# Optimization experiments

Measured on AMD Instinct MI355X. Metric: run time of the kernel, lower is better.

The kernel has to match this reference:

```python
import math
import jax, jax.numpy as jnp
import numpy as np


def _unskew(X):
    # X: B x M x (M+L)  ->  B x M x L (each row i shifted left by i)
    B, M, MpL = X.shape
    L = MpL - M
    X = X.reshape(B, M * MpL)
    X = jnp.pad(X, ((0, 0), (0, M)))          # B x (M*(M+L)+M)
    X = X.reshape(B, M, MpL + 1)               # B x M x (M+L+1)
    return X[:, :, :L]


def _skew(X, pad_value):
    # X: B x M x L  ->  B x M x (M+L) (each row i shifted right by i)
    B, M, L = X.shape
    X = jnp.pad(X, ((0, 0), (0, 0), (0, M + 1)), constant_values=pad_value)
    X = X.reshape(B, -1)[:, :-M]               # B x (M*(M+L))
    return X.reshape(B, M, M + L)


def setup_inputs() -> dict:
    key = jax.random.key(0)
    k1, k2, k3, k4 = jax.random.split(key, 4)
    B, M, L, H = 128, 512, 1024, 64   # B = batch*heads, key len = M+L
    query = jax.random.normal(k1, (B, M, H), dtype=jnp.float32)
    key_t = jax.random.normal(k2, (B, M + L, H), dtype=jnp.float32)
    value = jax.random.normal(k3, (B, M + L, H), dtype=jnp.float32)
    key_pe = jax.random.normal(k4, (1, H, L), dtype=jnp.float32) * 0.02
    return {"query": query, "key": key_t, "value": value, "key_pe": key_pe}


def reference(query, key, value, key_pe):
    H = query.shape[-1]  # head_dim
    # content attention: B x M x (M+L), then unskew to relative coords B x M x L
    attn_cont = jnp.einsum('bmh,bnh->bmn', query, key)
    attn_cont = _unskew(attn_cont)
    # position attention: B x M x L (key_pe broadcasts over batch)
    attn_pos = jnp.einsum('bmh,xhl->bml', query, key_pe)
    attn = (attn_cont + attn_pos) / math.sqrt(H)
    attn = jax.nn.softmax(attn, axis=-1)
    # dropout p=0.0 -> identity
    attn_sk = _skew(attn, 0.0)                  # B x M x (M+L)
    out = jnp.einsum('bmn,bnh->bmh', attn_sk, value)
    return out
```

## Files before the change

### kernel.cpp

```cpp
#include <hip/hip_runtime.h>
#include <math.h>

typedef __bf16 bf16x8 __attribute__((ext_vector_type(8)));
typedef __bf16 bf16x4 __attribute__((ext_vector_type(4)));
typedef float  f32x4  __attribute__((ext_vector_type(4)));

constexpr int B_  = 128;
constexpr int M_  = 512;
constexpr int L_  = 1024;
constexpr int H_  = 64;
constexpr int KL_ = 1536;

constexpr int BM = 64;
constexpr int KT = 64;
constexpr int NT = 17;
constexpr int KS = 72;
constexpr int PPS = 256;
constexpr int PSS = 40;

constexpr int OFF_KS   = 0;
constexpr int OFF_VT   = 18432;
constexpr int OFF_PPOS = 36864;
constexpr int OFF_PS   = 69632;
constexpr int SMEM_BYTES = 79872;
constexpr int OFF_OBUF = 0;
constexpr int OFF_LSUM = 18432;
constexpr int OBS = 36;

#define MFMA16(A, B, C) __builtin_amdgcn_mfma_f32_16x16x32_bf16((A), (B), (C), 0, 0, 0)

__global__ __launch_bounds__(256, 2)
void seqattn_v5(const float* __restrict__ Q, const float* __restrict__ K,
                const float* __restrict__ V, const float* __restrict__ PE,
                float* __restrict__ O) {
  __shared__ alignas(16) char smem[SMEM_BYTES];
  __bf16* ksb  = (__bf16*)(smem + OFF_KS);
  __bf16* vtb  = (__bf16*)(smem + OFF_VT);
  __bf16* ppos = (__bf16*)(smem + OFF_PPOS);

  const int tid  = threadIdx.x;
  const int w    = tid >> 6;
  const int lane = tid & 63;
  const int nid  = lane & 15;
  const int qid  = lane >> 4;
  const int a    = w >> 1;
  const int c    = w & 1;
  const int b    = blockIdx.x;
  const int m0   = blockIdx.y * BM;
  const int swz  = qid << 4;

  __bf16* ps = (__bf16*)(smem + OFF_PS) + w * 32 * PSS;

  bf16x8 aq[2][2];
  #pragma unroll
  for (int it = 0; it < 2; ++it) {
    const float* qg = &Q[((size_t)b * M_ + m0 + 32 * a + 16 * it + nid) * H_];
    #pragma unroll
    for (int j = 0; j < 8; ++j) {
      aq[it][0][j] = (__bf16)qg[8 * qid + j];
      aq[it][1][j] = (__bf16)qg[32 + 8 * qid + j];
    }
  }

  f32x4 o[2][4];
  float lpart[2][4];
  #pragma unroll
  for (int it = 0; it < 2; ++it) {
    #pragma unroll
    for (int ht = 0; ht < 4; ++ht) o[it][ht] = (f32x4){0.f, 0.f, 0.f, 0.f};
    #pragma unroll
    for (int r = 0; r < 4; ++r) lpart[it][r] = 0.f;
  }

  const int krow = tid >> 2,  khq = (tid & 3) * 16;
  const int vj = (tid & 15) * 4, vh = (tid >> 4) * 4;

  const float* peg = &PE[(size_t)(8 * qid) * L_ + 32 * c + nid];

  f32x4 kr[4], vr[4];
  {
    const float* kg = &K[((size_t)b * KL_ + m0 + krow) * H_ + khq];
    kr[0] = *(const f32x4*)kg;       kr[1] = *(const f32x4*)(kg + 4);
    kr[2] = *(const f32x4*)(kg + 8); kr[3] = *(const f32x4*)(kg + 12);
    const float* vg = &V[((size_t)b * KL_ + m0 + vj) * H_ + vh];
    #pragma unroll
    for (int e = 0; e < 4; ++e) vr[e] = *(const f32x4*)(vg + e * H_);
  }
  {
    const f32x4 z = {0.f, 0.f, 0.f, 0.f};
    #pragma unroll
    for (int nt = 0; nt < 2; ++nt) {
      bf16x8 b0, b1;
      #pragma unroll
      for (int j = 0; j < 8; ++j) {
        b0[j] = (__bf16)peg[(size_t)j * L_ + 16 * nt];
        b1[j] = (__bf16)peg[(size_t)(32 + j) * L_ + 16 * nt];
      }
      const int colb = 32 * c + 16 * nt + nid;
      #pragma unroll
      for (int it = 0; it < 2; ++it) {
        f32x4 pp = MFMA16(aq[it][0], b0, z);
        pp = MFMA16(aq[it][1], b1, pp);
        #pragma unroll
        for (int r = 0; r < 4; ++r)
          ppos[(32 * a + 16 * it + 4 * qid + r) * PPS + (colb ^ swz)] = (__bf16)pp[r];
      }
    }
  }
  {
    bf16x8 x0, x1;
    #pragma unroll
    for (int j = 0; j < 4; ++j) {
      x0[j] = (__bf16)kr[0][j]; x0[4 + j] = (__bf16)kr[1][j];
      x1[j] = (__bf16)kr[2][j]; x1[4 + j] = (__bf16)kr[3][j];
    }
    *(bf16x8*)&ksb[krow * KS + khq] = x0;
    *(bf16x8*)&ksb[krow * KS + khq + 8] = x1;
    #pragma unroll
    for (int e = 0; e < 4; ++e) {
      bf16x4 y = {(__bf16)vr[0][e], (__bf16)vr[1][e], (__bf16)vr[2][e], (__bf16)vr[3][e]};
      *(bf16x4*)&vtb[(vh + e) * KS + vj] = y;
    }
  }
  __syncthreads();

  for (int t = 0; t < NT; ++t) {
    if (t < 16) {
      const int j1 = m0 + KT * (t + 1);
      const float* kg = &K[((size_t)b * KL_ + j1 + krow) * H_ + khq];
      kr[0] = *(const f32x4*)kg;       kr[1] = *(const f32x4*)(kg + 4);
      kr[2] = *(const f32x4*)(kg + 8); kr[3] = *(const f32x4*)(kg + 12);
      const float* vg = &V[((size_t)b * KL_ + j1 + vj) * H_ + vh];
      #pragma unroll
      for (int e = 0; e < 4; ++e) vr[e] = *(const f32x4*)(vg + e * H_);
    }
    bf16x8 pf[2][2];
    const int ch = t + 1;
    if (t < 15) {
      const float* pc = peg + ch * 64;
      #pragma unroll
      for (int nt = 0; nt < 2; ++nt) {
        #pragma unroll
        for (int j = 0; j < 8; ++j) {
          pf[nt][0][j] = (__bf16)pc[(size_t)j * L_ + 16 * nt];
          pf[nt][1][j] = (__bf16)pc[(size_t)(32 + j) * L_ + 16 * nt];
        }
      }
    }

    const __bf16* kst = ksb + (t & 1) * 64 * KS;
    const __bf16* vtt = vtb + (t & 1) * 64 * KS;
    const f32x4 z = {0.f, 0.f, 0.f, 0.f};

    f32x4 s[2][2];
    #pragma unroll
    for (int nt = 0; nt < 2; ++nt) {
      const __bf16* kb = &kst[(32 * c + 16 * nt + nid) * KS];
      const bf16x8 b0 = *(const bf16x8*)&kb[8 * qid];
      const bf16x8 b1 = *(const bf16x8*)&kb[32 + 8 * qid];
      #pragma unroll
      for (int it = 0; it < 2; ++it) {
        s[it][nt] = MFMA16(aq[it][0], b0, z);
        s[it][nt] = MFMA16(aq[it][1], b1, s[it][nt]);
      }
    }

    if (t < 15) {
      #pragma unroll
      for (int nt = 0; nt < 2; ++nt) {
        const int colb = ((ch & 3) << 6) + 32 * c + 16 * nt + nid;
        #pragma unroll
        for (int it = 0; it < 2; ++it) {
          f32x4 pp = MFMA16(aq[it][0], pf[nt][0], z);
          pp = MFMA16(aq[it][1], pf[nt][1], pp);
          #pragma unroll
          for (int r = 0; r < 4; ++r)
            ppos[(32 * a + 16 * it + 4 * qid + r) * PPS + (colb ^ swz)] = (__bf16)pp[r];
        }
      }
    }

    const bool edge = (t == 0) || (t == 16);
    #pragma unroll
    for (int it = 0; it < 2; ++it) {
      #pragma unroll
      for (int r = 0; r < 4; ++r) {
        const int il = 32 * a + 16 * it + 4 * qid + r;
        const int rb = il * PPS;
        #pragma unroll
        for (int nt = 0; nt < 2; ++nt) {
          const int l = KT * t + 32 * c + 16 * nt + nid - il;
          float p;
          if (!edge || (unsigned)l < 1024u) {
            const float pe = (float)ppos[rb + ((l & 255) ^ swz)];
            p = __expf((s[it][nt][r] + pe) * 0.125f);
          } else {
            p = 0.f;
          }
          lpart[it][r] += p;
          ps[(16 * it + 4 * qid + r) * PSS + 16 * nt + nid] = (__bf16)p;
        }
      }
    }

    #pragma unroll
    for (int it = 0; it < 2; ++it) {
      const bf16x8 ap = *(const bf16x8*)&ps[(16 * it + nid) * PSS + 8 * qid];
      #pragma unroll
      for (int ht = 0; ht < 4; ++ht) {
        o[it][ht] = MFMA16(ap, *(const bf16x8*)&vtt[(16 * ht + nid) * KS + 32 * c + 8 * qid],
                           o[it][ht]);
      }
    }

    if (t < 16) {
      __bf16* ksn = ksb + ((t + 1) & 1) * 64 * KS;
      __bf16* vtn = vtb + ((t + 1) & 1) * 64 * KS;
      bf16x8 x0, x1;
      #pragma unroll
      for (int j = 0; j < 4; ++j) {
        x0[j] = (__bf16)kr[0][j]; x0[4 + j] = (__bf16)kr[1][j];
        x1[j] = (__bf16)kr[2][j]; x1[4 + j] = (__bf16)kr[3][j];
      }
      *(bf16x8*)&ksn[krow * KS + khq] = x0;
      *(bf16x8*)&ksn[krow * KS + khq + 8] = x1;
      #pragma unroll
      for (int e = 0; e < 4; ++e) {
        bf16x4 y = {(__bf16)vr[0][e], (__bf16)vr[1][e], (__bf16)vr[2][e], (__bf16)vr[3][e]};
        *(bf16x4*)&vtn[(vh + e) * KS + vj] = y;
      }
    }
    __syncthreads();
  }

  float* lsum = (float*)(smem + OFF_LSUM);
  float* obuf = (float*)(smem + OFF_OBUF);

  #pragma unroll
  for (int it = 0; it < 2; ++it) {
    #pragma unroll
    for (int r = 0; r < 4; ++r) {
      float v = lpart[it][r];
      v += __shfl_xor(v, 1); v += __shfl_xor(v, 2);
      v += __shfl_xor(v, 4); v += __shfl_xor(v, 8);
      lpart[it][r] = v;
    }
  }
  if (nid == 0) {
    #pragma unroll
    for (int it = 0; it < 2; ++it)
      #pragma unroll
      for (int r = 0; r < 4; ++r)
        lsum[c * 64 + 32 * a + 16 * it + 4 * qid + r] = lpart[it][r];
  }
  if (c == 1) {
    #pragma unroll
    for (int it = 0; it < 2; ++it)
      #pragma unroll
      for (int ht = 0; ht < 4; ++ht)
        *(f32x4*)&obuf[(a * 64 + 16 * ht + nid) * OBS + 16 * it + 4 * qid] = o[it][ht];
  }
  __syncthreads();
  if (c == 0) {
    float inv[2][4];
    #pragma unroll
    for (int it = 0; it < 2; ++it)
      #pragma unroll
      for (int r = 0; r < 4; ++r) {
        const int row = 32 * a + 16 * it + 4 * qid + r;
        inv[it][r] = 1.f / (lsum[row] + lsum[64 + row]);
      }
    #pragma unroll
    for (int it = 0; it < 2; ++it) {
      #pragma unroll
      for (int ht = 0; ht < 4; ++ht) {
        f32x4 oo = o[it][ht] +
                   *(const f32x4*)&obuf[(a * 64 + 16 * ht + nid) * OBS + 16 * it + 4 * qid];
        #pragma unroll
        for (int r = 0; r < 4; ++r) {
          const int row = 32 * a + 16 * it + 4 * qid + r;
          O[((size_t)b * M_ + m0 + row) * H_ + 16 * ht + nid] = oo[r] * inv[it][r];
        }
      }
    }
  }
}

extern "C" void kernel_launch(void* const* d_in, const int* in_sizes, int n_in,
                              void* d_out, int out_size, void* d_ws, size_t ws_size,
                              hipStream_t stream) {
  const float* Q  = (const float*)d_in[0];
  const float* K  = (const float*)d_in[1];
  const float* V  = (const float*)d_in[2];
  const float* PE = (const float*)d_in[3];
  float* O = (float*)d_out;

  dim3 grid(B_, M_ / BM);
  hipLaunchKernelGGL(seqattn_v5, grid, dim3(256), 0, stream, Q, K, V, PE, O);
}
```

Baseline: 221.2 us.

## Compute transposed scores to keep softmax probabilities in registers for PV MFMA

Swaps the MFMA operand order so score tiles come out transposed, which puts each lane's probabilities in the layout the 16x16x16 bf16 MFMA A-operand expects. That removes the shared-memory round trip for P. K is now loaded straight from global into registers instead of being staged through LDS. The position table is stored pre-shifted with a new swizzle so it can be read as bf16x4 vectors. The smaller LDS footprint allows raising launch bounds to 3 blocks per CU, at the cost of more register pressure and less-coalesced K loads.

```diff
diff --git a/kernel.cpp b/kernel.cpp
--- a/kernel.cpp
+++ b/kernel.cpp
@@ -4,6 +4,7 @@
 typedef __bf16 bf16x8 __attribute__((ext_vector_type(8)));
 typedef __bf16 bf16x4 __attribute__((ext_vector_type(4)));
 typedef float  f32x4  __attribute__((ext_vector_type(4)));
+typedef short  s16x4  __attribute__((ext_vector_type(4)));
 
 constexpr int B_  = 128;
 constexpr int M_  = 512;
@@ -11,30 +12,31 @@
 constexpr int H_  = 64;
 constexpr int KL_ = 1536;
 
-constexpr int BM = 64;
-constexpr int KT = 64;
-constexpr int NT = 17;
-constexpr int KS = 72;
+constexpr int BM  = 64;
+constexpr int KT  = 64;
+constexpr int NT  = 17;
+constexpr int KS  = 72;
 constexpr int PPS = 256;
-constexpr int PSS = 40;
-
-constexpr int OFF_KS   = 0;
-constexpr int OFF_VT   = 18432;
-constexpr int OFF_PPOS = 36864;
-constexpr int OFF_PS   = 69632;
-constexpr int SMEM_BYTES = 79872;
+
+constexpr int OFF_VT   = 0;
+constexpr int OFF_PPOS = 18432;
+constexpr int SMEM_BYTES = 51200;
 constexpr int OFF_OBUF = 0;
 constexpr int OFF_LSUM = 18432;
 constexpr int OBS = 36;
 
-#define MFMA16(A, B, C) __builtin_amdgcn_mfma_f32_16x16x32_bf16((A), (B), (C), 0, 0, 0)
-
-__global__ __launch_bounds__(256, 2)
-void seqattn_v5(const float* __restrict__ Q, const float* __restrict__ K,
+#define MFMA32(A, B, C) __builtin_amdgcn_mfma_f32_16x16x32_bf16((A), (B), (C), 0, 0, 0)
+
+static __device__ __forceinline__ f32x4 mfma_pv(bf16x4 a, bf16x4 b, f32x4 c) {
+  return __builtin_amdgcn_mfma_f32_16x16x16bf16_1k(
+      __builtin_bit_cast(s16x4, a), __builtin_bit_cast(s16x4, b), c, 0, 0, 0);
+}
+
+__global__ __launch_bounds__(256, 3)
+void seqattn_v6(const float* __restrict__ Q, const float* __restrict__ K,
                 const float* __restrict__ V, const float* __restrict__ PE,
                 float* __restrict__ O) {
   __shared__ alignas(16) char smem[SMEM_BYTES];
-  __bf16* ksb  = (__bf16*)(smem + OFF_KS);
   __bf16* vtb  = (__bf16*)(smem + OFF_VT);
   __bf16* ppos = (__bf16*)(smem + OFF_PPOS);
 
@@ -47,9 +49,7 @@
   const int c    = w & 1;
   const int b    = blockIdx.x;
   const int m0   = blockIdx.y * BM;
-  const int swz  = qid << 4;
-
-  __bf16* ps = (__bf16*)(smem + OFF_PS) + w * 32 * PSS;
+  const int swzn = (nid & 7) << 2;
 
   bf16x8 aq[2][2];
   #pragma unroll
@@ -63,172 +63,186 @@
   }
 
   f32x4 o[2][4];
-  float lpart[2][4];
-  #pragma unroll
-  for (int it = 0; it < 2; ++it) {
+  float lpart[2] = {0.f, 0.f};
+  #pragma unroll
+  for (int it = 0; it < 2; ++it)
     #pragma unroll
     for (int ht = 0; ht < 4; ++ht) o[it][ht] = (f32x4){0.f, 0.f, 0.f, 0.f};
-    #pragma unroll
-    for (int r = 0; r < 4; ++r) lpart[it][r] = 0.f;
-  }
-
-  const int krow = tid >> 2,  khq = (tid & 3) * 16;
+
   const int vj = (tid & 15) * 4, vh = (tid >> 4) * 4;
 
   const float* peg = &PE[(size_t)(8 * qid) * L_ + 32 * c + nid];
 
-  f32x4 kr[4], vr[4];
+  bf16x8 ak[2][2];
+  #pragma unroll
+  for (int nt = 0; nt < 2; ++nt) {
+    const float* kg = &K[((size_t)b * KL_ + m0 + 32 * c + 16 * nt + nid) * H_ + 8 * qid];
+    const f32x4 k0 = *(const f32x4*)kg;
+    const f32x4 k1 = *(const f32x4*)(kg + 4);
+    const f32x4 k2 = *(const f32x4*)(kg + 32);
+    const f32x4 k3 = *(const f32x4*)(kg + 36);
+    #pragma unroll
+    for (int j = 0; j < 4; ++j) {
+      ak[nt][0][j] = (__bf16)k0[j]; ak[nt][0][4 + j] = (__bf16)k1[j];
+      ak[nt][1][j] = (__bf16)k2[j]; ak[nt][1][4 + j] = (__bf16)k3[j];
+    }
+  }
+  f32x4 vr[4];
   {
-    const float* kg = &K[((size_t)b * KL_ + m0 + krow) * H_ + khq];
-    kr[0] = *(const f32x4*)kg;       kr[1] = *(const f32x4*)(kg + 4);
-    kr[2] = *(const f32x4*)(kg + 8); kr[3] = *(const f32x4*)(kg + 12);
     const float* vg = &V[((size_t)b * KL_ + m0 + vj) * H_ + vh];
     #pragma unroll
     for (int e = 0; e < 4; ++e) vr[e] = *(const f32x4*)(vg + e * H_);
   }
   {
     const f32x4 z = {0.f, 0.f, 0.f, 0.f};
+    bf16x8 pf0[2][2];
+    #pragma unroll
+    for (int nt = 0; nt < 2; ++nt)
+      #pragma unroll
+      for (int j = 0; j < 8; ++j) {
+        pf0[nt][0][j] = (__bf16)peg[(size_t)j * L_ + 16 * nt];
+        pf0[nt][1][j] = (__bf16)peg[(size_t)(32 + j) * L_ + 16 * nt];
+      }
     #pragma unroll
     for (int nt = 0; nt < 2; ++nt) {
-      bf16x8 b0, b1;
-      #pragma unroll
-      for (int j = 0; j < 8; ++j) {
-        b0[j] = (__bf16)peg[(size_t)j * L_ + 16 * nt];
-        b1[j] = (__bf16)peg[(size_t)(32 + j) * L_ + 16 * nt];
-      }
-      const int colb = 32 * c + 16 * nt + nid;
       #pragma unroll
       for (int it = 0; it < 2; ++it) {
-        f32x4 pp = MFMA16(aq[it][0], b0, z);
-        pp = MFMA16(aq[it][1], b1, pp);
+        f32x4 pp = MFMA32(pf0[nt][0], aq[it][0], z);
+        pp = MFMA32(pf0[nt][1], aq[it][1], pp);
+        const int row = 32 * a + 16 * it + nid;
+        const int cb  = 32 * c + 16 * nt + 4 * qid + row;
         #pragma unroll
         for (int r = 0; r < 4; ++r)
-          ppos[(32 * a + 16 * it + 4 * qid + r) * PPS + (colb ^ swz)] = (__bf16)pp[r];
-      }
-    }
-  }
-  {
-    bf16x8 x0, x1;
-    #pragma unroll
-    for (int j = 0; j < 4; ++j) {
-      x0[j] = (__bf16)kr[0][j]; x0[4 + j] = (__bf16)kr[1][j];
-      x1[j] = (__bf16)kr[2][j]; x1[4 + j] = (__bf16)kr[3][j];
-    }
-    *(bf16x8*)&ksb[krow * KS + khq] = x0;
-    *(bf16x8*)&ksb[krow * KS + khq + 8] = x1;
-    #pragma unroll
-    for (int e = 0; e < 4; ++e) {
-      bf16x4 y = {(__bf16)vr[0][e], (__bf16)vr[1][e], (__bf16)vr[2][e], (__bf16)vr[3][e]};
-      *(bf16x4*)&vtb[(vh + e) * KS + vj] = y;
-    }
+          ppos[row * PPS + (((cb + r) & 255) ^ swzn)] = (__bf16)pp[r];
+      }
+    }
+  }
+  #pragma unroll
+  for (int e = 0; e < 4; ++e) {
+    bf16x4 y = {(__bf16)vr[0][e], (__bf16)vr[1][e], (__bf16)vr[2][e], (__bf16)vr[3][e]};
+    *(bf16x4*)&vtb[(vh + e) * KS + vj] = y;
   }
   __syncthreads();
 
   for (int t = 0; t < NT; ++t) {
+    bf16x4 pe4[2][2];
+    #pragma unroll
+    for (int it = 0; it < 2; ++it) {
+      const int row = 32 * a + 16 * it + nid;
+      #pragma unroll
+      for (int nt = 0; nt < 2; ++nt)
+        pe4[it][nt] = *(const bf16x4*)
+            &ppos[row * PPS + ((64 * (t & 3) + 32 * c + 16 * nt + 4 * qid) ^ swzn)];
+    }
+
+    bf16x8 akn[2][2];
     if (t < 16) {
       const int j1 = m0 + KT * (t + 1);
-      const float* kg = &K[((size_t)b * KL_ + j1 + krow) * H_ + khq];
-      kr[0] = *(const f32x4*)kg;       kr[1] = *(const f32x4*)(kg + 4);
-      kr[2] = *(const f32x4*)(kg + 8); kr[3] = *(const f32x4*)(kg + 12);
+      #pragma unroll
+      for (int nt = 0; nt < 2; ++nt) {
+        const float* kg = &K[((size_t)b * KL_ + j1 + 32 * c + 16 * nt + nid) * H_ + 8 * qid];
+        const f32x4 k0 = *(const f32x4*)kg;
+        const f32x4 k1 = *(const f32x4*)(kg + 4);
+        const f32x4 k2 = *(const f32x4*)(kg + 32);
+        const f32x4 k3 = *(const f32x4*)(kg + 36);
+        #pragma unroll
+        for (int j = 0; j < 4; ++j) {
+          akn[nt][0][j] = (__bf16)k0[j]; akn[nt][0][4 + j] = (__bf16)k1[j];
+          akn[nt][1][j] = (__bf16)k2[j]; akn[nt][1][4 + j] = (__bf16)k3[j];
+        }
+      }
       const float* vg = &V[((size_t)b * KL_ + j1 + vj) * H_ + vh];
       #pragma unroll
       for (int e = 0; e < 4; ++e) vr[e] = *(const f32x4*)(vg + e * H_);
     }
     bf16x8 pf[2][2];
-    const int ch = t + 1;
     if (t < 15) {
-      const float* pc = peg + ch * 64;
-      #pragma unroll
-      for (int nt = 0; nt < 2; ++nt) {
+      const float* pc = peg + (t + 1) * 64;
+      #pragma unroll
+      for (int nt = 0; nt < 2; ++nt)
         #pragma unroll
         for (int j = 0; j < 8; ++j) {
           pf[nt][0][j] = (__bf16)pc[(size_t)j * L_ + 16 * nt];
           pf[nt][1][j] = (__bf16)pc[(size_t)(32 + j) * L_ + 16 * nt];
         }
-      }
-    }
-
-    const __bf16* kst = ksb + (t & 1) * 64 * KS;
+    }
+
     const __bf16* vtt = vtb + (t & 1) * 64 * KS;
     const f32x4 z = {0.f, 0.f, 0.f, 0.f};
 
     f32x4 s[2][2];
     #pragma unroll
-    for (int nt = 0; nt < 2; ++nt) {
-      const __bf16* kb = &kst[(32 * c + 16 * nt + nid) * KS];
-      const bf16x8 b0 = *(const bf16x8*)&kb[8 * qid];
-      const bf16x8 b1 = *(const bf16x8*)&kb[32 + 8 * qid];
+    for (int nt = 0; nt < 2; ++nt)
       #pragma unroll
       for (int it = 0; it < 2; ++it) {
-        s[it][nt] = MFMA16(aq[it][0], b0, z);
-        s[it][nt] = MFMA16(aq[it][1], b1, s[it][nt]);
-      }
-    }
+        s[it][nt] = MFMA32(ak[nt][0], aq[it][0], z);
+        s[it][nt] = MFMA32(ak[nt][1], aq[it][1], s[it][nt]);
+      }
 
     if (t < 15) {
+      const int chb = 64 * ((t + 1) & 3);
       #pragma unroll
       for (int nt = 0; nt < 2; ++nt) {
-        const int colb = ((ch & 3) << 6) + 32 * c + 16 * nt + nid;
         #pragma unroll
         for (int it = 0; it < 2; ++it) {
-          f32x4 pp = MFMA16(aq[it][0], pf[nt][0], z);
-          pp = MFMA16(aq[it][1], pf[nt][1], pp);
+          f32x4 pp = MFMA32(pf[nt][0], aq[it][0], z);
+          pp = MFMA32(pf[nt][1], aq[it][1], pp);
+          const int row = 32 * a + 16 * it + nid;
+          const int cb  = chb + 32 * c + 16 * nt + 4 * qid + row;
           #pragma unroll
           for (int r = 0; r < 4; ++r)
-            ppos[(32 * a + 16 * it + 4 * qid + r) * PPS + (colb ^ swz)] = (__bf16)pp[r];
+            ppos[row * PPS + (((cb + r) & 255) ^ swzn)] = (__bf16)pp[r];
         }
       }
     }
 
     const bool edge = (t == 0) || (t == 16);
+    bf16x4 pa[2][2];
     #pragma unroll
     for (int it = 0; it < 2; ++it) {
-      #pragma unroll
-      for (int r = 0; r < 4; ++r) {
-        const int il = 32 * a + 16 * it + 4 * qid + r;
-        const int rb = il * PPS;
-        #pragma unroll
-        for (int nt = 0; nt < 2; ++nt) {
-          const int l = KT * t + 32 * c + 16 * nt + nid - il;
+      const int row = 32 * a + 16 * it + nid;
+      #pragma unroll
+      for (int nt = 0; nt < 2; ++nt) {
+        const int lb = KT * t + 32 * c + 16 * nt + 4 * qid - row;
+        #pragma unroll
+        for (int r = 0; r < 4; ++r) {
+          const int l = lb + r;
           float p;
-          if (!edge || (unsigned)l < 1024u) {
-            const float pe = (float)ppos[rb + ((l & 255) ^ swz)];
-            p = __expf((s[it][nt][r] + pe) * 0.125f);
-          } else {
+          if (!edge || (unsigned)l < 1024u)
+            p = __expf((s[it][nt][r] + (float)pe4[it][nt][r]) * 0.125f);
+          else
             p = 0.f;
-          }
-          lpart[it][r] += p;
-          ps[(16 * it + 4 * qid + r) * PSS + 16 * nt + nid] = (__bf16)p;
-        }
-      }
-    }
-
-    #pragma unroll
-    for (int it = 0; it < 2; ++it) {
-      const bf16x8 ap = *(const bf16x8*)&ps[(16 * it + nid) * PSS + 8 * qid];
-      #pragma unroll
-      for (int ht = 0; ht < 4; ++ht) {
-        o[it][ht] = MFMA16(ap, *(const bf16x8*)&vtt[(16 * ht + nid) * KS + 32 * c + 8 * qid],
-                           o[it][ht]);
-      }
+          lpart[it] += p;
+          pa[it][nt][r] = (__bf16)p;
+        }
+      }
+    }
+
+    #pragma unroll
+    for (int nt = 0; nt < 2; ++nt) {
+      bf16x4 vb[4];
+      #pragma unroll
+      for (int ht = 0; ht < 4; ++ht)
+        vb[ht] = *(const bf16x4*)&vtt[(16 * ht + nid) * KS + 32 * c + 16 * nt + 4 * qid];
+      #pragma unroll
+      for (int it = 0; it < 2; ++it)
+        #pragma unroll
+        for (int ht = 0; ht < 4; ++ht)
+          o[it][ht] = mfma_pv(pa[it][nt], vb[ht], o[it][ht]);
     }
 
     if (t < 16) {
-      __bf16* ksn = ksb + ((t + 1) & 1) * 64 * KS;
       __bf16* vtn = vtb + ((t + 1) & 1) * 64 * KS;
-      bf16x8 x0, x1;
-      #pragma unroll
-      for (int j = 0; j < 4; ++j) {
-        x0[j] = (__bf16)kr[0][j]; x0[4 + j] = (__bf16)kr[1][j];
-        x1[j] = (__bf16)kr[2][j]; x1[4 + j] = (__bf16)kr[3][j];
-      }
-      *(bf16x8*)&ksn[krow * KS + khq] = x0;
-      *(bf16x8*)&ksn[krow * KS + khq + 8] = x1;
       #pragma unroll
       for (int e = 0; e < 4; ++e) {
         bf16x4 y = {(__bf16)vr[0][e], (__bf16)vr[1][e], (__bf16)vr[2][e], (__bf16)vr[3][e]};
         *(bf16x4*)&vtn[(vh + e) * KS + vj] = y;
       }
+      #pragma unroll
+      for (int nt = 0; nt < 2; ++nt) {
+        ak[nt][0] = akn[nt][0];
+        ak[nt][1] = akn[nt][1];
+      }
     }
     __syncthreads();
   }
@@ -238,20 +252,15 @@
 
   #pragma unroll
   for (int it = 0; it < 2; ++it) {
-    #pragma unroll
-    for (int r = 0; r < 4; ++r) {
-      float v = lpart[it][r];
-      v += __shfl_xor(v, 1); v += __shfl_xor(v, 2);
-      v += __shfl_xor(v, 4); v += __shfl_xor(v, 8);
-      lpart[it][r] = v;
-    }
-  }
-  if (nid == 0) {
+    float v = lpart[it];
+    v += __shfl_xor(v, 16);
+    v += __shfl_xor(v, 32);
+    lpart[it] = v;
+  }
+  if (qid == 0) {
     #pragma unroll
     for (int it = 0; it < 2; ++it)
-      #pragma unroll
-      for (int r = 0; r < 4; ++r)
-        lsum[c * 64 + 32 * a + 16 * it + 4 * qid + r] = lpart[it][r];
+      lsum[c * 64 + 32 * a + 16 * it + nid] = lpart[it];
   }
   if (c == 1) {
     #pragma unroll
@@ -296,5 +305,5 @@
   float* O = (float*)d_out;
 
   dim3 grid(B_, M_ / BM);
-  hipLaunchKernelGGL(seqattn_v5, grid, dim3(256), 0, stream, Q, K, V, PE, O);
+  hipLaunchKernelGGL(seqattn_v6, grid, dim3(256), 0, stream, Q, K, V, PE, O);
 }
```

New measurement: 319.3 us. 44.4% more time.
